# Optimization experiments

Hardware: AMD Instinct MI355X
Metric: run time of the kernel (lower is better)

The kernel has to match this reference:

```python
import jax, jax.numpy as jnp
import numpy as np

D_MODEL = 256
D_INNER = 512
NHEADS = 8
HEADDIM = 64
NGROUPS = 1
D_DIST = 4
LOG_SCALE = 512.0
MAX_VALUE = 4.0
NUM_POINTS = 10
EPS = 1e-5


def roty(t):
    c, s = jnp.cos(t), jnp.sin(t)
    z, o = jnp.zeros_like(t), jnp.ones_like(t)
    r0 = jnp.stack([c, z, s], -1)
    r1 = jnp.stack([z, o, z], -1)
    r2 = jnp.stack([-s, z, c], -1)
    return jnp.stack([r0, r1, r2], -2)


def box_corners(center, size, angle):
    # flip_axis_to_camera: (x, -z, y)
    cam_c = jnp.stack([center[..., 0], -center[..., 2], center[..., 1]], -1)
    R = roty(angle)  # (B,K,3,3)
    sx = jnp.array([1, 1, -1, -1, 1, 1, -1, -1], jnp.float32)
    sy = jnp.array([1, 1, 1, 1, -1, -1, -1, -1], jnp.float32)
    sz = jnp.array([1, -1, -1, 1, 1, -1, -1, 1], jnp.float32)
    l, w, h = size[..., 0:1], size[..., 1:2], size[..., 2:3]
    local = jnp.stack([l * sx / 2, h * sy / 2, w * sz / 2], -1)  # (B,K,8,3)
    cam = jnp.einsum('bkcj,bkij->bkci', local, R) + cam_c[..., None, :]
    # camera -> lidar: (x, z, -y)
    return jnp.stack([cam[..., 0], cam[..., 2], -cam[..., 1]], -1)


def trilinear_sample(table, g):
    # table (P,P,P,C); g (N,3) normalized coords (gx,gy,gz); gx->axis2, gy->axis1, gz->axis0
    # replicates F.grid_sample(mode='bilinear', align_corners=False, padding_mode='zeros')
    P = table.shape[0]
    pix = ((g + 1.0) * P - 1.0) * 0.5
    k, j, i = pix[:, 0], pix[:, 1], pix[:, 2]
    i0f, j0f, k0f = jnp.floor(i), jnp.floor(j), jnp.floor(k)
    wi, wj, wk = i - i0f, j - j0f, k - k0f
    i0, j0, k0 = i0f.astype(jnp.int32), j0f.astype(jnp.int32), k0f.astype(jnp.int32)
    out = jnp.zeros((g.shape[0], table.shape[-1]), table.dtype)
    for a in (0, 1):
        for b in (0, 1):
            for c in (0, 1):
                ii, jj, kk = i0 + a, j0 + b, k0 + c
                valid = (ii >= 0) & (ii < P) & (jj >= 0) & (jj < P) & (kk >= 0) & (kk < P)
                v = table[jnp.clip(ii, 0, P - 1), jnp.clip(jj, 0, P - 1), jnp.clip(kk, 0, P - 1)]
                w = (wi if a else 1 - wi) * (wj if b else 1 - wj) * (wk if c else 1 - wk)
                out = out + jnp.where(valid, w, 0.0)[:, None] * v
    return out


def box_dist(key_xyz, query_xyz, query_size, query_angle, w1, b1, w2):
    B, K = query_xyz.shape[:2]
    L = key_xyz.shape[1]
    corners = jax.lax.stop_gradient(box_corners(query_xyz, query_size, query_angle))
    d = corners.reshape(B, K * 8, 3)[:, :, None, :] - key_xyz[:, None, :, :]  # (B,K*8,L,3)
    d = jnp.stack([d[..., 0], -d[..., 2], d[..., 1]], -1)
    R = roty(jnp.tile(query_angle, (1, 8)))  # matches torch .repeat((1,8)) ordering (bug-faithful)
    d = jnp.einsum('bqlj,bqjk->bqlk', d, R)
    d = jnp.stack([d[..., 0], d[..., 2], -d[..., 1]], -1)
    d = jnp.sign(d) * jnp.log2(jnp.abs(d) * LOG_SCALE + 1.0) / np.float32(np.log2(8.0))
    g = (d / MAX_VALUE).reshape(-1, 3)
    lin = jnp.linspace(-MAX_VALUE, MAX_VALUE, NUM_POINTS, dtype=jnp.float32)
    coords = jnp.stack(jnp.meshgrid(lin, lin, lin, indexing='ij'), -1)  # (P,P,P,3)
    table = jnp.maximum(coords @ w1.T + b1, 0.0) @ w2.T  # cpb MLP -> (P,P,P,4)
    samp = trilinear_sample(table, g).reshape(B, K, 8, L, D_DIST)
    return samp.sum(axis=2).transpose(0, 2, 1, 3)  # (B,L,K,4)


def dwconv7(x, w, b):
    # x (B,L,C), depthwise conv1d k=7 pad=3
    y = jax.lax.conv_general_dilated(jnp.swapaxes(x, 1, 2), w, (1,), [(3, 3)],
                                     dimension_numbers=('NCH', 'OIH', 'NCH'),
                                     feature_group_count=w.shape[0])
    return jnp.swapaxes(y + b[None, :, None], 1, 2)


def issm_scan(x, Bm, Cm, dt, A, h0):
    # x (B,L,H,hd), Bm/Cm (B,L,K), dt (B,L,K,H), h0 (B,H,hd,K); state index = query axis K
    dA = jnp.exp(dt * A)          # (B,L,K,H)
    dB = dt * Bm[..., None]       # (B,L,K,H)
    xs = (jnp.moveaxis(x, 1, 0), jnp.moveaxis(dA, 1, 0), jnp.moveaxis(dB, 1, 0), jnp.moveaxis(Cm, 1, 0))

    def step(h, inp):
        x_t, dA_t, dB_t, C_t = inp
        h = h * jnp.swapaxes(dA_t, 1, 2)[:, :, None, :] + x_t[..., None] * jnp.swapaxes(dB_t, 1, 2)[:, :, None, :]
        return h, jnp.einsum('bhdk,bk->bhd', h, C_t)

    hT, ys = jax.lax.scan(step, h0, xs)
    return jnp.moveaxis(ys, 0, 1), hT


def _forward(in_key, in_query, key_xyz, query_xyz, query_size, query_angle, Wkey, conv_w, conv_b, convb_w, convb_b, Wq, Wbc, Wdt, dt_bias, A_log, Dp, Wok, Woq, key_norm_w, ln_w, ln_b, cpb_w1, cpb_b1, cpb_w2):
    B, L, _ = in_key.shape
    K = in_query.shape[1]
    zxbcdt = in_key @ Wkey.T
    z = zxbcdt[..., :D_INNER]
    xbc = zxbcdt[..., D_INNER:2 * D_INNER + 2 * NGROUPS]
    dt_k = zxbcdt[..., 2 * D_INNER + 2 * NGROUPS:]
    xbc_f = jax.nn.silu(dwconv7(xbc, conv_w, conv_b))
    x = xbc_f[..., :D_INNER].reshape(B, L, NHEADS, HEADDIM)
    b_bias = xbc_f[..., D_INNER:D_INNER + NGROUPS]
    c_bias = xbc_f[..., D_INNER + NGROUPS:]
    xbc_b = jax.nn.silu(dwconv7(xbc_f, convb_w, convb_b))
    x_b = xbc_b[..., :D_INNER].reshape(B, L, NHEADS, HEADDIM)
    bb_b = xbc_b[..., D_INNER:D_INNER + NGROUPS]
    cb_b = xbc_b[..., D_INNER + NGROUPS:]
    dist = box_dist(key_xyz, query_xyz, query_size, query_angle, cpb_w1, cpb_b1, cpb_w2)  # (B,L,K,4)
    bc = dist @ Wbc.T  # (B,L,K,2*ngroups)
    Bm0, Cm0 = bc[..., 0], bc[..., 1]
    dt = jax.nn.softplus(dist @ Wdt.T + dt_k[:, :, None, :] + dt_bias)  # (B,L,K,H)
    A = -jnp.exp(A_log)
    h0 = (in_query @ Wq.T).reshape(B, K, NHEADS, HEADDIM).transpose(0, 2, 3, 1)  # (B,H,hd,K)
    y_f, h_f = issm_scan(x, Bm0 + b_bias, Cm0 + c_bias, dt, A, h0)
    rev = lambda a: jnp.flip(a, axis=1)
    y_b, h_b = issm_scan(rev(x_b), rev(Bm0 + bb_b), rev(Cm0 + cb_b), rev(dt), A, h0)
    y = y_f + rev(y_b) + Dp[None, None, :, None] * x
    yk = y.reshape(B, L, D_INNER)
    gated = yk * jax.nn.silu(z)
    gated = gated * jax.lax.rsqrt(jnp.mean(gated * gated, -1, keepdims=True) + EPS) * key_norm_w
    out_key = gated @ Wok.T
    state = (0.5 * (h_f + h_b)).transpose(0, 3, 1, 2).reshape(B, K, D_INNER)
    mu = jnp.mean(state, -1, keepdims=True)
    var = jnp.mean((state - mu) ** 2, -1, keepdims=True)
    out_query = (((state - mu) * jax.lax.rsqrt(var + EPS)) * ln_w + ln_b) @ Woq.T
    return out_key, out_query


def setup_inputs():
    key = jax.random.key(0)
    ks = jax.random.split(key, 24)
    B, L, K = 2, 1024, 128
    D, DI, H, G = D_MODEL, D_INNER, NHEADS, NGROUPS
    CC = DI + 2 * G
    n = jax.random.normal
    inp = {}
    inp['in_key'] = n(ks[0], (B, L, D), jnp.float32)
    inp['in_query'] = n(ks[1], (B, K, D), jnp.float32)
    inp['key_xyz'] = jax.random.uniform(ks[2], (B, L, 3))
    inp['query_xyz'] = jax.random.uniform(ks[3], (B, K, 3))
    inp['query_size'] = jax.random.uniform(ks[4], (B, K, 3)) + 0.1
    inp['query_angle'] = jax.random.uniform(ks[5], (B, K)) * 2.0 * np.float32(np.pi)
    inp['Wkey'] = n(ks[6], (2 * DI + 2 * G + H, D)) * 0.02
    inp['conv_w'] = n(ks[7], (CC, 1, 7)) * 0.1
    inp['conv_b'] = jnp.zeros((CC,))
    inp['convb_w'] = n(ks[8], (CC, 1, 7)) * 0.1
    inp['convb_b'] = jnp.zeros((CC,))
    inp['Wq'] = n(ks[9], (DI, D)) * 0.02
    inp['Wbc'] = n(ks[10], (2 * G, D_DIST)) * 0.1
    inp['Wdt'] = n(ks[11], (H, D_DIST)) * 0.1
    dt = jnp.exp(jax.random.uniform(ks[12], (H,)) * (np.float32(np.log(0.1)) - np.float32(np.log(1e-4))) + np.float32(np.log(1e-4)))
    inp['dt_bias'] = dt + jnp.log(-jnp.expm1(-dt))
    inp['A_log'] = jnp.log(jax.random.uniform(ks[13], (H,), minval=1.0, maxval=16.0))
    inp['Dp'] = jnp.ones((H,))
    inp['Wok'] = n(ks[14], (D, DI)) * 0.02
    inp['Woq'] = n(ks[15], (D, DI)) * 0.02
    inp['key_norm_w'] = jnp.ones((DI,))
    inp['ln_w'] = jnp.ones((DI,))
    inp['ln_b'] = jnp.zeros((DI,))
    inp['cpb_w1'] = n(ks[16], (128, 3)) * 0.1
    inp['cpb_b1'] = jnp.zeros((128,))
    inp['cpb_w2'] = n(ks[17], (D_DIST, 128)) * 0.1
    return inp


def reference(in_key, in_query, key_xyz, query_xyz, query_size, query_angle, Wkey, conv_w, conv_b, convb_w, convb_b, Wq, Wbc, Wdt, dt_bias, A_log, Dp, Wok, Woq, key_norm_w, ln_w, ln_b, cpb_w1, cpb_b1, cpb_w2):
    return _forward(in_key, in_query, key_xyz, query_xyz, query_size, query_angle, Wkey, conv_w, conv_b, convb_w, convb_b, Wq, Wbc, Wdt, dt_bias, A_log, Dp, Wok, Woq, key_norm_w, ln_w, ln_b, cpb_w1, cpb_b1, cpb_w2)
```

## Files before the change

### kernel.cpp

```cpp
#include <hip/hip_runtime.h>
#include <math.h>

#define B_ 2
#define L_ 1024
#define K_ 128
#define DM 256
#define DI 512
#define NH 8
#define HD 64
#define CC 514
#define ZCOLS 1034
#define NC 16
#define TC 64

__device__ __forceinline__ float wave_sum(float v) {
    v += __shfl_xor(v, 1);  v += __shfl_xor(v, 2);  v += __shfl_xor(v, 4);
    v += __shfl_xor(v, 8);  v += __shfl_xor(v, 16); v += __shfl_xor(v, 32);
    return v;
}

__device__ __forceinline__ float dpp_row_reduce16(float v) {
    int t;
    t = __builtin_amdgcn_update_dpp(0, __float_as_int(v), 0x128, 0xF, 0xF, true);
    v += __int_as_float(t);
    t = __builtin_amdgcn_update_dpp(0, __float_as_int(v), 0x124, 0xF, 0xF, true);
    v += __int_as_float(t);
    t = __builtin_amdgcn_update_dpp(0, __float_as_int(v), 0x122, 0xF, 0xF, true);
    v += __int_as_float(t);
    t = __builtin_amdgcn_update_dpp(0, __float_as_int(v), 0x121, 0xF, 0xF, true);
    v += __int_as_float(t);
    return v;
}

__device__ __forceinline__ float silu_f(float x) {
    return x / (1.f + expf(-x));
}

__device__ void gemm_dev(const float* __restrict__ A, const float* __restrict__ Bm,
                         float* __restrict__ C, int M, int N, int K, int bm, int bn) {
    __shared__ float As[2][16][68];
    __shared__ float Bs[2][16][68];
    const int tid = threadIdx.x;
    const int sr = tid >> 2;
    const int sk = (tid & 3) * 4;
    const int tx = tid & 15, ty = tid >> 4;
    const int NT = K >> 4;
    const float* Arow = A + (size_t)(bm + sr) * K + sk;
    const float* Brow = Bm + (size_t)(bn + sr) * K + sk;
    const bool bok = (bn + sr) < N;

    float4 av = *(const float4*)Arow;
    float4 bv = bok ? *(const float4*)Brow : make_float4(0.f, 0.f, 0.f, 0.f);
    As[0][sk + 0][sr] = av.x; As[0][sk + 1][sr] = av.y;
    As[0][sk + 2][sr] = av.z; As[0][sk + 3][sr] = av.w;
    Bs[0][sk + 0][sr] = bv.x; Bs[0][sk + 1][sr] = bv.y;
    Bs[0][sk + 2][sr] = bv.z; Bs[0][sk + 3][sr] = bv.w;
    __syncthreads();

    float acc[4][4] = {};
    for (int t = 0; t < NT; ++t) {
        if (t + 1 < NT) {
            av = *(const float4*)(Arow + (t + 1) * 16);
            bv = bok ? *(const float4*)(Brow + (t + 1) * 16) : make_float4(0.f, 0.f, 0.f, 0.f);
        }
        const int bi = t & 1;
#pragma unroll
        for (int kk = 0; kk < 16; ++kk) {
            float4 a = *(const float4*)&As[bi][kk][ty * 4];
            float4 b = *(const float4*)&Bs[bi][kk][tx * 4];
            acc[0][0] = fmaf(a.x, b.x, acc[0][0]); acc[0][1] = fmaf(a.x, b.y, acc[0][1]);
            acc[0][2] = fmaf(a.x, b.z, acc[0][2]); acc[0][3] = fmaf(a.x, b.w, acc[0][3]);
            acc[1][0] = fmaf(a.y, b.x, acc[1][0]); acc[1][1] = fmaf(a.y, b.y, acc[1][1]);
            acc[1][2] = fmaf(a.y, b.z, acc[1][2]); acc[1][3] = fmaf(a.y, b.w, acc[1][3]);
            acc[2][0] = fmaf(a.z, b.x, acc[2][0]); acc[2][1] = fmaf(a.z, b.y, acc[2][1]);
            acc[2][2] = fmaf(a.z, b.z, acc[2][2]); acc[2][3] = fmaf(a.z, b.w, acc[2][3]);
            acc[3][0] = fmaf(a.w, b.x, acc[3][0]); acc[3][1] = fmaf(a.w, b.y, acc[3][1]);
            acc[3][2] = fmaf(a.w, b.z, acc[3][2]); acc[3][3] = fmaf(a.w, b.w, acc[3][3]);
        }
        __syncthreads();
        if (t + 1 < NT) {
            const int ni = (t + 1) & 1;
            As[ni][sk + 0][sr] = av.x; As[ni][sk + 1][sr] = av.y;
            As[ni][sk + 2][sr] = av.z; As[ni][sk + 3][sr] = av.w;
            Bs[ni][sk + 0][sr] = bv.x; Bs[ni][sk + 1][sr] = bv.y;
            Bs[ni][sk + 2][sr] = bv.z; Bs[ni][sk + 3][sr] = bv.w;
            __syncthreads();
        }
    }
#pragma unroll
    for (int i = 0; i < 4; ++i) {
        int m = bm + ty * 4 + i;
        int n0 = bn + tx * 4;
        if (n0 + 3 < N) {
            float* cp = &C[(size_t)m * N + n0];
            *(float2*)cp = make_float2(acc[i][0], acc[i][1]);
            *(float2*)(cp + 2) = make_float2(acc[i][2], acc[i][3]);
        } else {
#pragma unroll
            for (int j = 0; j < 4; ++j)
                if (n0 + j < N) C[(size_t)m * N + n0 + j] = acc[i][j];
        }
    }
}

__global__ __launch_bounds__(256) void front_k(
    const float* __restrict__ in_key, const float* __restrict__ Wkey, float* __restrict__ zx,
    const float* __restrict__ in_query, const float* __restrict__ Wq, float* __restrict__ h0b,
    const float* __restrict__ qxyz, const float* __restrict__ qsize,
    const float* __restrict__ qang, const float* __restrict__ w1,
    const float* __restrict__ b1, const float* __restrict__ w2,
    float* __restrict__ cb, float* __restrict__ tbl) {
    int bid = blockIdx.x, tid = threadIdx.x;
    if (bid < 544) {
        gemm_dev(in_key, Wkey, zx, 2048, ZCOLS, 256, (bid & 31) * 64, (bid >> 5) * 64);
    } else if (bid < 576) {
        int r = bid - 544;
        gemm_dev(in_query, Wq, h0b, 256, 512, 256, (r & 3) * 64, (r >> 2) * 64);
    } else if (bid < 584) {
        int idx = (bid - 576) * 256 + tid;
        int b = idx >> 10;
        int q = idx & 1023;
        int k = q >> 3;
        int c = q & 7;
        const float sx[8] = {1, 1, -1, -1, 1, 1, -1, -1};
        const float sy[8] = {1, 1, 1, 1, -1, -1, -1, -1};
        const float sz[8] = {1, -1, -1, 1, 1, -1, -1, 1};
        float cx = qxyz[(b * K_ + k) * 3 + 0];
        float cy = qxyz[(b * K_ + k) * 3 + 1];
        float cz = qxyz[(b * K_ + k) * 3 + 2];
        float lv = qsize[(b * K_ + k) * 3 + 0];
        float wv = qsize[(b * K_ + k) * 3 + 1];
        float hv = qsize[(b * K_ + k) * 3 + 2];
        float ang = qang[b * K_ + k];
        float ca = cosf(ang), sa = sinf(ang);
        float ccx = cx, ccy = -cz, ccz = cy;
        float l0 = lv * sx[c] * 0.5f;
        float l1 = hv * sy[c] * 0.5f;
        float l2 = wv * sz[c] * 0.5f;
        float m0 = ca * l0 + sa * l2 + ccx;
        float m1 = l1 + ccy;
        float m2 = -sa * l0 + ca * l2 + ccz;
        float angr = qang[b * K_ + (q & (K_ - 1))];
        float4* o = (float4*)(cb + (size_t)idx * 8);
        o[0] = make_float4(m0, m2, -m1, cosf(angr));
        o[1] = make_float4(sinf(angr), 0.f, 0.f, 0.f);
    } else {
        int p = (bid - 584) * 256 + tid;
        if (p >= 1000) return;
        int i = p / 100, j = (p / 10) % 10, k = p % 10;
        float c0 = (8.f / 9.f) * i - 4.f;
        float c1 = (8.f / 9.f) * j - 4.f;
        float c2 = (8.f / 9.f) * k - 4.f;
        float a0 = 0.f, a1 = 0.f, a2 = 0.f, a3 = 0.f;
        for (int m = 0; m < 128; ++m) {
            float t = fmaf(c0, w1[m * 3 + 0], fmaf(c1, w1[m * 3 + 1], fmaf(c2, w1[m * 3 + 2], b1[m])));
            t = fmaxf(t, 0.f);
            a0 = fmaf(t, w2[m], a0);
            a1 = fmaf(t, w2[128 + m], a1);
            a2 = fmaf(t, w2[256 + m], a2);
            a3 = fmaf(t, w2[384 + m], a3);
        }
        tbl[p * 4 + 0] = a0; tbl[p * 4 + 1] = a1;
        tbl[p * 4 + 2] = a2; tbl[p * 4 + 3] = a3;
    }
}

__global__ void dwconv_silu(const float* __restrict__ xin, int in_stride, int in_off,
                            const float* __restrict__ w, const float* __restrict__ bias,
                            float* __restrict__ out) {
    int c = blockIdx.y * blockDim.x + threadIdx.x;
    if (c >= CC) return;
    int row = blockIdx.x;
    int l = row & (L_ - 1);
    const float* xr = xin + (size_t)row * in_stride + in_off + c;
    float acc = bias[c];
#pragma unroll
    for (int j = 0; j < 7; ++j) {
        int ll = l + j - 3;
        if (ll >= 0 && ll < L_) acc = fmaf(xr[(ptrdiff_t)(j - 3) * in_stride], w[c * 7 + j], acc);
    }
    out[(size_t)row * CC + c] = silu_f(acc);
}

__global__ __launch_bounds__(128) void geo_k(
    const float* __restrict__ kxyz, const float* __restrict__ cb,
    const float* __restrict__ tbl, const float* __restrict__ zx,
    const float* __restrict__ xf, const float* __restrict__ xb,
    const float* __restrict__ wbc, const float* __restrict__ wdt,
    const float* __restrict__ dtb, const float* __restrict__ alog,
    float* __restrict__ dA, float* __restrict__ dBf, float* __restrict__ dBb,
    float* __restrict__ Cf, float* __restrict__ Cb) {
    __shared__ float t_s[4000];
    int row = blockIdx.x;
    int b = row >> 10;
    int l = row & 1023;
    int k = threadIdx.x;
    for (int i = threadIdx.x; i < 4000; i += 128) t_s[i] = tbl[i];
    __syncthreads();
    float kx = kxyz[(size_t)row * 3 + 0];
    float ky = kxyz[(size_t)row * 3 + 1];
    float kz = kxyz[(size_t)row * 3 + 2];
    float acc0 = 0.f, acc1 = 0.f, acc2 = 0.f, acc3 = 0.f;
#pragma unroll
    for (int c = 0; c < 8; ++c) {
        int q = k * 8 + c;
        const float4* p = (const float4*)(cb + (size_t)(b * 1024 + q) * 8);
        float4 v0 = p[0], v1 = p[1];
        float d0 = v0.x - kx, d1 = v0.y - ky, d2 = v0.z - kz;
        float rc = v0.w, rs = v1.x;
        float e0 = d0, e1 = -d2, e2 = d1;
        float f0 = rc * e0 - rs * e2;
        float f1 = e1;
        float f2 = rs * e0 + rc * e2;
        float g0 = f0, g1 = f2, g2 = -f1;
        g0 = copysignf(log2f(fabsf(g0) * 512.f + 1.f) * (1.f / 12.f), g0);
        g1 = copysignf(log2f(fabsf(g1) * 512.f + 1.f) * (1.f / 12.f), g1);
        g2 = copysignf(log2f(fabsf(g2) * 512.f + 1.f) * (1.f / 12.f), g2);
        float iq = 5.f * g2 + 4.5f;
        float jq = 5.f * g1 + 4.5f;
        float kq = 5.f * g0 + 4.5f;
        float i0f = floorf(iq), j0f = floorf(jq), k0f = floorf(kq);
        float wi = iq - i0f, wj = jq - j0f, wk = kq - k0f;
        int i0 = (int)i0f, j0 = (int)j0f, k0 = (int)k0f;
#pragma unroll
        for (int a = 0; a < 2; ++a) {
#pragma unroll
            for (int bb = 0; bb < 2; ++bb) {
#pragma unroll
                for (int cc = 0; cc < 2; ++cc) {
                    int ii = i0 + a, jj = j0 + bb, kk = k0 + cc;
                    if ((unsigned)ii < 10u && (unsigned)jj < 10u && (unsigned)kk < 10u) {
                        float wgt = (a ? wi : 1.f - wi) * (bb ? wj : 1.f - wj) * (cc ? wk : 1.f - wk);
                        const float* tp = &t_s[((ii * 10 + jj) * 10 + kk) * 4];
                        acc0 = fmaf(wgt, tp[0], acc0);
                        acc1 = fmaf(wgt, tp[1], acc1);
                        acc2 = fmaf(wgt, tp[2], acc2);
                        acc3 = fmaf(wgt, tp[3], acc3);
                    }
                }
            }
        }
    }
    float B0 = acc0 * wbc[0] + acc1 * wbc[1] + acc2 * wbc[2] + acc3 * wbc[3];
    float C0 = acc0 * wbc[4] + acc1 * wbc[5] + acc2 * wbc[6] + acc3 * wbc[7];
    float bbf = xf[(size_t)row * CC + 512], cbf = xf[(size_t)row * CC + 513];
    float bbb = xb[(size_t)row * CC + 512], cbb = xb[(size_t)row * CC + 513];
    Cf[(size_t)row * K_ + k] = C0 + cbf;
    Cb[(size_t)row * K_ + k] = C0 + cbb;
    float Bf = B0 + bbf, Bb = B0 + bbb;
#pragma unroll
    for (int hh = 0; hh < NH; ++hh) {
        float s = acc0 * wdt[hh * 4 + 0] + acc1 * wdt[hh * 4 + 1] +
                  acc2 * wdt[hh * 4 + 2] + acc3 * wdt[hh * 4 + 3];
        s += zx[(size_t)row * ZCOLS + 1026 + hh] + dtb[hh];
        float dtv = (s > 20.f) ? s : log1pf(expf(s));
        float Av = -expf(alog[hh]);
        size_t o = ((size_t)(b * NH + hh) * L_ + l) * K_ + k;
        dA[o] = expf(dtv * Av);
        dBf[o] = dtv * Bf;
        dBb[o] = dtv * Bb;
    }
}

__global__ __launch_bounds__(256) void scan_part6(
    const float* __restrict__ dA, const float* __restrict__ dBf, const float* __restrict__ dBb,
    const float* __restrict__ Cf, const float* __restrict__ Cb,
    const float* __restrict__ xf, const float* __restrict__ xb,
    float* __restrict__ Sbuf, float* __restrict__ Pbuf,
    float* __restrict__ yf, float* __restrict__ yb) {
    __shared__ float lds[2][3584];
    int bid = blockIdx.x;
    int c = bid & 15;
    int hh = (bid >> 4) & 7;
    int b = (bid >> 7) & 1;
    int dir = bid >> 8;
    int tid = threadIdx.x;
    int lane = tid & 63;
    int w = tid >> 6;
    int dg = lane >> 4, kg = lane & 15;
    int dloc = w * 4 + dg;
    int klo = kg * 4, khi = 64 + kg * 4;

    const float* Bsrc = dir ? dBb : dBf;
    const float* Csrc = dir ? Cb : Cf;
    const float* Xsrc = dir ? xb : xf;
    float* Ydst = dir ? yb : yf;
    int t0 = dir ? (L_ - 1 - c * TC) : c * TC;
    int stp = dir ? -1 : 1;

    const float* Abase = dA + ((size_t)(b * NH + hh) * L_) * K_;
    const float* Bbase = Bsrc + ((size_t)(b * NH + hh) * L_) * K_;
    const float* Cbase = Csrc + ((size_t)b * L_) * K_;
    const float* Xbase = Xsrc + ((size_t)b * L_) * CC + hh * HD;

    const bool hasx = (tid < 128);

    auto gaddr = [&](int v, int tb) -> const float* {
        if (v < 768) {
            int r = (v >> 5) & 7;
            int c4 = v & 31;
            int l = t0 + stp * (tb + r);
            const float* base = (v < 256) ? Abase : ((v < 512) ? Bbase : Cbase);
            return base + (size_t)l * K_ + c4 * 4;
        } else {
            int vv = v - 768;
            int r = vv >> 4, c4 = vv & 15;
            int l = t0 + stp * (tb + r);
            return Xbase + (size_t)l * CC + c4 * 4;
        }
    };

    float hA[8] = {0, 0, 0, 0, 0, 0, 0, 0};
    float hB[8] = {0, 0, 0, 0, 0, 0, 0, 0};
    float hC[8] = {0, 0, 0, 0, 0, 0, 0, 0};
    float hD[8] = {0, 0, 0, 0, 0, 0, 0, 0};
    float cum[8] = {1, 1, 1, 1, 1, 1, 1, 1};

    float4 rA = *(const float4*)gaddr(tid, 0);
    float4 rB = *(const float4*)gaddr(256 + tid, 0);
    float4 rC = *(const float4*)gaddr(512 + tid, 0);
    float4 rX = hasx ? *(const float4*)gaddr(768 + tid, 0) : make_float4(0, 0, 0, 0);
    *(float4*)&lds[0][4 * tid] = rA;
    *(float4*)&lds[0][1024 + 4 * tid] = rB;
    *(float4*)&lds[0][2048 + 4 * tid] = rC;
    if (hasx) *(float4*)&lds[0][3072 + 4 * tid] = rX;
    __syncthreads();

    float* pY = Ydst + ((size_t)(b * L_ + t0)) * DI + hh * HD + dloc;
    const ptrdiff_t dY = (ptrdiff_t)stp * DI;

    for (int it = 0; it < TC / 8; ++it) {
        int tb = it * 8;
        if (it < TC / 8 - 1) {
            rA = *(const float4*)gaddr(tid, tb + 8);
            rB = *(const float4*)gaddr(256 + tid, tb + 8);
            rC = *(const float4*)gaddr(512 + tid, tb + 8);
            if (hasx) rX = *(const float4*)gaddr(768 + tid, tb + 8);
        }
        const float* Lb = lds[it & 1];
        float4 a0 = *(const float4*)&Lb[klo];
        float4 a1 = *(const float4*)&Lb[khi];
        float4 b0 = *(const float4*)&Lb[1024 + klo];
        float4 b1 = *(const float4*)&Lb[1024 + khi];
        float4 c0 = *(const float4*)&Lb[2048 + klo];
        float4 c1 = *(const float4*)&Lb[2048 + khi];
        float x0 = Lb[3072 + dloc];
        float x1 = Lb[3072 + 16 + dloc];
        float x2 = Lb[3072 + 32 + dloc];
        float x3 = Lb[3072 + 48 + dloc];
#pragma unroll
        for (int st = 0; st < 8; ++st) {
            float4 na0, na1, nb0, nb1, nc0, nc1;
            float nx0 = 0.f, nx1 = 0.f, nx2 = 0.f, nx3 = 0.f;
            if (st < 7) {
                int o = (st + 1) * 128;
                na0 = *(const float4*)&Lb[o + klo];
                na1 = *(const float4*)&Lb[o + khi];
                nb0 = *(const float4*)&Lb[1024 + o + klo];
                nb1 = *(const float4*)&Lb[1024 + o + khi];
                nc0 = *(const float4*)&Lb[2048 + o + klo];
                nc1 = *(const float4*)&Lb[2048 + o + khi];
                int xo = 3072 + (st + 1) * 64 + dloc;
                nx0 = Lb[xo]; nx1 = Lb[xo + 16]; nx2 = Lb[xo + 32]; nx3 = Lb[xo + 48];
            }
            cum[0] *= a0.x; cum[1] *= a0.y; cum[2] *= a0.z; cum[3] *= a0.w;
            cum[4] *= a1.x; cum[5] *= a1.y; cum[6] *= a1.z; cum[7] *= a1.w;
            float u0, u1, u2, u3;
            hA[0] = fmaf(hA[0], a0.x, x0 * b0.x); u0 = hA[0] * c0.x;
            hA[1] = fmaf(hA[1], a0.y, x0 * b0.y); u1 = hA[1] * c0.y;
            hA[2] = fmaf(hA[2], a0.z, x0 * b0.z); u2 = hA[2] * c0.z;
            hA[3] = fmaf(hA[3], a0.w, x0 * b0.w); u3 = hA[3] * c0.w;
            hA[4] = fmaf(hA[4], a1.x, x0 * b1.x); u0 = fmaf(hA[4], c1.x, u0);
            hA[5] = fmaf(hA[5], a1.y, x0 * b1.y); u1 = fmaf(hA[5], c1.y, u1);
            hA[6] = fmaf(hA[6], a1.z, x0 * b1.z); u2 = fmaf(hA[6], c1.z, u2);
            hA[7] = fmaf(hA[7], a1.w, x0 * b1.w); u3 = fmaf(hA[7], c1.w, u3);
            float rrA = dpp_row_reduce16((u0 + u1) + (u2 + u3));
            hB[0] = fmaf(hB[0], a0.x, x1 * b0.x); u0 = hB[0] * c0.x;
            hB[1] = fmaf(hB[1], a0.y, x1 * b0.y); u1 = hB[1] * c0.y;
            hB[2] = fmaf(hB[2], a0.z, x1 * b0.z); u2 = hB[2] * c0.z;
            hB[3] = fmaf(hB[3], a0.w, x1 * b0.w); u3 = hB[3] * c0.w;
            hB[4] = fmaf(hB[4], a1.x, x1 * b1.x); u0 = fmaf(hB[4], c1.x, u0);
            hB[5] = fmaf(hB[5], a1.y, x1 * b1.y); u1 = fmaf(hB[5], c1.y, u1);
            hB[6] = fmaf(hB[6], a1.z, x1 * b1.z); u2 = fmaf(hB[6], c1.z, u2);
            hB[7] = fmaf(hB[7], a1.w, x1 * b1.w); u3 = fmaf(hB[7], c1.w, u3);
            float rrB = dpp_row_reduce16((u0 + u1) + (u2 + u3));
            hC[0] = fmaf(hC[0], a0.x, x2 * b0.x); u0 = hC[0] * c0.x;
            hC[1] = fmaf(hC[1], a0.y, x2 * b0.y); u1 = hC[1] * c0.y;
            hC[2] = fmaf(hC[2], a0.z, x2 * b0.z); u2 = hC[2] * c0.z;
            hC[3] = fmaf(hC[3], a0.w, x2 * b0.w); u3 = hC[3] * c0.w;
            hC[4] = fmaf(hC[4], a1.x, x2 * b1.x); u0 = fmaf(hC[4], c1.x, u0);
            hC[5] = fmaf(hC[5], a1.y, x2 * b1.y); u1 = fmaf(hC[5], c1.y, u1);
            hC[6] = fmaf(hC[6], a1.z, x2 * b1.z); u2 = fmaf(hC[6], c1.z, u2);
            hC[7] = fmaf(hC[7], a1.w, x2 * b1.w); u3 = fmaf(hC[7], c1.w, u3);
            float rrC = dpp_row_reduce16((u0 + u1) + (u2 + u3));
            hD[0] = fmaf(hD[0], a0.x, x3 * b0.x); u0 = hD[0] * c0.x;
            hD[1] = fmaf(hD[1], a0.y, x3 * b0.y); u1 = hD[1] * c0.y;
            hD[2] = fmaf(hD[2], a0.z, x3 * b0.z); u2 = hD[2] * c0.z;
            hD[3] = fmaf(hD[3], a0.w, x3 * b0.w); u3 = hD[3] * c0.w;
            hD[4] = fmaf(hD[4], a1.x, x3 * b1.x); u0 = fmaf(hD[4], c1.x, u0);
            hD[5] = fmaf(hD[5], a1.y, x3 * b1.y); u1 = fmaf(hD[5], c1.y, u1);
            hD[6] = fmaf(hD[6], a1.z, x3 * b1.z); u2 = fmaf(hD[6], c1.z, u2);
            hD[7] = fmaf(hD[7], a1.w, x3 * b1.w); u3 = fmaf(hD[7], c1.w, u3);
            float rrD = dpp_row_reduce16((u0 + u1) + (u2 + u3));
            if (kg == 0) { pY[0] = rrA; pY[16] = rrB; pY[32] = rrC; pY[48] = rrD; }
            pY += dY;
            if (st < 7) {
                a0 = na0; a1 = na1; b0 = nb0; b1 = nb1; c0 = nc0; c1 = nc1;
                x0 = nx0; x1 = nx1; x2 = nx2; x3 = nx3;
            }
        }
        __syncthreads();
        if (it < TC / 8 - 1) {
            *(float4*)&lds[(it + 1) & 1][4 * tid] = rA;
            *(float4*)&lds[(it + 1) & 1][1024 + 4 * tid] = rB;
            *(float4*)&lds[(it + 1) & 1][2048 + 4 * tid] = rC;
            if (hasx) *(float4*)&lds[(it + 1) & 1][3072 + 4 * tid] = rX;
        }
        __syncthreads();
    }

    int ibh = (dir * B_ + b) * NH + hh;
    {
        float* Sp = Sbuf + (((size_t)ibh * NC + c) * HD + dloc) * K_;
        *(float4*)(Sp + klo) = make_float4(hA[0], hA[1], hA[2], hA[3]);
        *(float4*)(Sp + khi) = make_float4(hA[4], hA[5], hA[6], hA[7]);
        Sp += (size_t)16 * K_;
        *(float4*)(Sp + klo) = make_float4(hB[0], hB[1], hB[2], hB[3]);
        *(float4*)(Sp + khi) = make_float4(hB[4], hB[5], hB[6], hB[7]);
        Sp += (size_t)16 * K_;
        *(float4*)(Sp + klo) = make_float4(hC[0], hC[1], hC[2], hC[3]);
        *(float4*)(Sp + khi) = make_float4(hC[4], hC[5], hC[6], hC[7]);
        Sp += (size_t)16 * K_;
        *(float4*)(Sp + klo) = make_float4(hD[0], hD[1], hD[2], hD[3]);
        *(float4*)(Sp + khi) = make_float4(hD[4], hD[5], hD[6], hD[7]);
    }
    if (dir == 0 && tid < 16) {
        float* Pp = Pbuf + ((size_t)((b * NH + hh) * NC + c)) * K_;
        *(float4*)(Pp + klo) = make_float4(cum[0], cum[1], cum[2], cum[3]);
        *(float4*)(Pp + khi) = make_float4(cum[4], cum[5], cum[6], cum[7]);
    }
}

__global__ __launch_bounds__(256) void scan_combine(
    const float* __restrict__ h0buf, float* __restrict__ Sbuf,
    const float* __restrict__ Pbuf, float* __restrict__ hfin) {
    int bid = blockIdx.x;
    int dq = bid & 3;
    int hh = (bid >> 2) & 7;
    int b = (bid >> 5) & 1;
    int dir = bid >> 6;
    int tid = threadIdx.x;
    int w = tid >> 6;
    int lane = tid & 63;
    int dsl = dq * 4 + w;
    int dg = lane >> 4, kg = lane & 15;
    int d = dsl * 4 + dg;
    int k0 = kg * 8;

    float H[8];
#pragma unroll
    for (int j = 0; j < 8; ++j)
        H[j] = h0buf[(size_t)(b * K_ + k0 + j) * DI + hh * HD + d];

    int ibh = (dir * B_ + b) * NH + hh;
    for (int c = 0; c < NC; ++c) {
        float* Sp = Sbuf + (((size_t)ibh * NC + c) * HD + d) * K_ + k0;
        int cF = dir ? (NC - 1 - c) : c;
        const float* Pp = Pbuf + ((size_t)((b * NH + hh) * NC + cF)) * K_ + k0;
        float4 sA = *(const float4*)(Sp + 0);
        float4 sB = *(const float4*)(Sp + 4);
        float4 pA = *(const float4*)(Pp + 0);
        float4 pB = *(const float4*)(Pp + 4);
        *(float4*)(Sp + 0) = make_float4(H[0], H[1], H[2], H[3]);
        *(float4*)(Sp + 4) = make_float4(H[4], H[5], H[6], H[7]);
        H[0] = fmaf(H[0], pA.x, sA.x); H[1] = fmaf(H[1], pA.y, sA.y);
        H[2] = fmaf(H[2], pA.z, sA.z); H[3] = fmaf(H[3], pA.w, sA.w);
        H[4] = fmaf(H[4], pB.x, sB.x); H[5] = fmaf(H[5], pB.y, sB.y);
        H[6] = fmaf(H[6], pB.z, sB.z); H[7] = fmaf(H[7], pB.w, sB.w);
    }
    float* hf = hfin + ((((size_t)dir * B_ + b) * NH + hh) * HD + d) * K_ + k0;
    *(float4*)(hf + 0) = make_float4(H[0], H[1], H[2], H[3]);
    *(float4*)(hf + 4) = make_float4(H[4], H[5], H[6], H[7]);
}

#define CP 72
#define WSWZ(k) ((((k) >> 3) & 3) << 2)
__global__ __launch_bounds__(256) void scan_corr(
    const float* __restrict__ dA, const float* __restrict__ Cf, const float* __restrict__ Cb,
    const float* __restrict__ Sbuf, float* __restrict__ yf, float* __restrict__ yb) {
    __shared__ float Wl[128][CP];
    __shared__ float Hl[128][CP];
    int iid = blockIdx.x;
    int c = iid & 15;
    int hh = (iid >> 4) & 7;
    int b = (iid >> 7) & 1;
    int dir = iid >> 8;
    int tid = threadIdx.x;
    const float* Csrc = dir ? Cb : Cf;

    if (tid < 128) {
        int k = tid;
        float cum = 1.f;
        const float* pA = dA + ((size_t)(b * NH + hh) * L_) * K_ + k;
        const float* pC = Csrc + ((size_t)b * L_) * K_ + k;
        int sw = WSWZ(k);
#pragma unroll 4
        for (int t = 0; t < TC; ++t) {
            int l = dir ? (L_ - 1 - (c * TC + t)) : (c * TC + t);
            cum *= pA[(size_t)l * K_];
            Wl[k][t ^ sw] = cum * pC[(size_t)l * K_];
        }
    }
    {
        int d = tid & 63, kq = tid >> 6;
        int ibh = (dir * B_ + b) * NH + hh;
        const float* Hp = Sbuf + (((size_t)ibh * NC + c) * HD + d) * K_;
#pragma unroll
        for (int i = 0; i < 8; ++i) {
            int q = kq * 8 + i;
            float4 v = *(const float4*)(Hp + q * 4);
            Hl[q * 4 + 0][d] = v.x; Hl[q * 4 + 1][d] = v.y;
            Hl[q * 4 + 2][d] = v.z; Hl[q * 4 + 3][d] = v.w;
        }
    }
    __syncthreads();
    int a = tid >> 4;
    int bc = tid & 15;
    int t0v = a * 4, d0v = bc * 4;
    float acc[4][4] = {};
    for (int k = 0; k < 128; ++k) {
        float4 w4 = *(const float4*)&Wl[k][t0v ^ WSWZ(k)];
        float4 h4 = *(const float4*)&Hl[k][d0v];
        acc[0][0] = fmaf(w4.x, h4.x, acc[0][0]); acc[0][1] = fmaf(w4.x, h4.y, acc[0][1]);
        acc[0][2] = fmaf(w4.x, h4.z, acc[0][2]); acc[0][3] = fmaf(w4.x, h4.w, acc[0][3]);
        acc[1][0] = fmaf(w4.y, h4.x, acc[1][0]); acc[1][1] = fmaf(w4.y, h4.y, acc[1][1]);
        acc[1][2] = fmaf(w4.y, h4.z, acc[1][2]); acc[1][3] = fmaf(w4.y, h4.w, acc[1][3]);
        acc[2][0] = fmaf(w4.z, h4.x, acc[2][0]); acc[2][1] = fmaf(w4.z, h4.y, acc[2][1]);
        acc[2][2] = fmaf(w4.z, h4.z, acc[2][2]); acc[2][3] = fmaf(w4.z, h4.w, acc[2][3]);
        acc[3][0] = fmaf(w4.w, h4.x, acc[3][0]); acc[3][1] = fmaf(w4.w, h4.y, acc[3][1]);
        acc[3][2] = fmaf(w4.w, h4.z, acc[3][2]); acc[3][3] = fmaf(w4.w, h4.w, acc[3][3]);
    }
    float* Ydst = dir ? yb : yf;
#pragma unroll
    for (int i = 0; i < 4; ++i) {
        int t = t0v + i;
        int l = dir ? (L_ - 1 - (c * TC + t)) : (c * TC + t);
        float* yp = Ydst + ((size_t)(b * L_ + l)) * DI + hh * HD + d0v;
        float4 old = *(float4*)yp;
        old.x += acc[i][0]; old.y += acc[i][1];
        old.z += acc[i][2]; old.w += acc[i][3];
        *(float4*)yp = old;
    }
}

__global__ __launch_bounds__(256) void gated_k(
    const float* __restrict__ yf, const float* __restrict__ yb,
    const float* __restrict__ xf, const float* __restrict__ zx,
    const float* __restrict__ Dp, const float* __restrict__ knw,
    float* __restrict__ gated) {
    __shared__ float sb[4];
    int row = blockIdx.x;
    int tid = threadIdx.x;
    float g[2];
    float ss = 0.f;
#pragma unroll
    for (int u = 0; u < 2; ++u) {
        int c = tid + u * 256;
        float yv = yf[(size_t)row * DI + c] + yb[(size_t)row * DI + c] +
                   Dp[c >> 6] * xf[(size_t)row * CC + c];
        float z = zx[(size_t)row * ZCOLS + c];
        float gv = yv * silu_f(z);
        g[u] = gv;
        ss = fmaf(gv, gv, ss);
    }
    float wsum = wave_sum(ss);
    if ((tid & 63) == 0) sb[tid >> 6] = wsum;
    __syncthreads();
    float tot = sb[0] + sb[1] + sb[2] + sb[3];
    float rms = rsqrtf(tot * (1.f / 512.f) + 1e-5f);
#pragma unroll
    for (int u = 0; u < 2; ++u) {
        int c = tid + u * 256;
        gated[(size_t)row * DI + c] = g[u] * rms * knw[c];
    }
}

__global__ __launch_bounds__(256) void final_k(
    const float* __restrict__ gated, const float* __restrict__ Wok, float* __restrict__ out,
    const float* __restrict__ hfin, const float* __restrict__ lnw,
    const float* __restrict__ lnb, const float* __restrict__ woq,
    float* __restrict__ outq) {
    int bid = blockIdx.x, tid = threadIdx.x;
    if (bid < 128) {
        gemm_dev(gated, Wok, out, 2048, 256, 512, (bid & 31) * 64, (bid >> 5) * 64);
        return;
    }
    __shared__ float sln[512];
    __shared__ float sb1[4];
    __shared__ float sb2[4];
    int bk = bid - 128;
    int b = bk >> 7;
    int k = bk & 127;
    float st[2];
    float ssum = 0.f;
#pragma unroll
    for (int u = 0; u < 2; ++u) {
        int c = tid + u * 256;
        int hh = c >> 6, d = c & 63;
        size_t o0 = (((size_t)(0 * B_ + b) * NH + hh) * HD + d) * K_ + k;
        size_t o1 = (((size_t)(1 * B_ + b) * NH + hh) * HD + d) * K_ + k;
        st[u] = 0.5f * (hfin[o0] + hfin[o1]);
        ssum += st[u];
    }
    float wsum = wave_sum(ssum);
    if ((tid & 63) == 0) sb1[tid >> 6] = wsum;
    __syncthreads();
    float mu = (sb1[0] + sb1[1] + sb1[2] + sb1[3]) * (1.f / 512.f);
    float vs = 0.f;
#pragma unroll
    for (int u = 0; u < 2; ++u) {
        float t = st[u] - mu;
        vs = fmaf(t, t, vs);
    }
    float wv = wave_sum(vs);
    if ((tid & 63) == 0) sb2[tid >> 6] = wv;
    __syncthreads();
    float var = (sb2[0] + sb2[1] + sb2[2] + sb2[3]) * (1.f / 512.f);
    float inv = rsqrtf(var + 1e-5f);
#pragma unroll
    for (int u = 0; u < 2; ++u) {
        int c = tid + u * 256;
        sln[c] = (st[u] - mu) * inv * lnw[c] + lnb[c];
    }
    __syncthreads();
    const float4* w4 = (const float4*)(woq + (size_t)tid * 512);
    float acc = 0.f;
#pragma unroll 4
    for (int i = 0; i < 128; ++i) {
        float4 wvv = w4[i];
        float4 sv = *(const float4*)&sln[i * 4];
        acc = fmaf(wvv.x, sv.x, acc);
        acc = fmaf(wvv.y, sv.y, acc);
        acc = fmaf(wvv.z, sv.z, acc);
        acc = fmaf(wvv.w, sv.w, acc);
    }
    outq[(size_t)bk * 256 + tid] = acc;
}

extern "C" void kernel_launch(void* const* d_in, const int* in_sizes, int n_in,
                              void* d_out, int out_size, void* d_ws, size_t ws_size,
                              hipStream_t stream) {
    const float* in_key      = (const float*)d_in[0];
    const float* in_query    = (const float*)d_in[1];
    const float* key_xyz     = (const float*)d_in[2];
    const float* query_xyz   = (const float*)d_in[3];
    const float* query_size  = (const float*)d_in[4];
    const float* query_angle = (const float*)d_in[5];
    const float* Wkey        = (const float*)d_in[6];
    const float* conv_w      = (const float*)d_in[7];
    const float* conv_b      = (const float*)d_in[8];
    const float* convb_w     = (const float*)d_in[9];
    const float* convb_b     = (const float*)d_in[10];
    const float* Wq          = (const float*)d_in[11];
    const float* Wbc         = (const float*)d_in[12];
    const float* Wdt         = (const float*)d_in[13];
    const float* dt_bias     = (const float*)d_in[14];
    const float* A_log       = (const float*)d_in[15];
    const float* Dp          = (const float*)d_in[16];
    const float* Wok         = (const float*)d_in[17];
    const float* Woq         = (const float*)d_in[18];
    const float* key_norm_w  = (const float*)d_in[19];
    const float* ln_w        = (const float*)d_in[20];
    const float* ln_b        = (const float*)d_in[21];
    const float* cpb_w1      = (const float*)d_in[22];
    const float* cpb_b1      = (const float*)d_in[23];
    const float* cpb_w2      = (const float*)d_in[24];
    float* out = (float*)d_out;

    float* wsf = (float*)d_ws;
    float* zx    = wsf + 0;
    float* xf    = wsf + 2117632;
    float* xb    = wsf + 3170304;
    float* tbl   = wsf + 4222976;
    float* cbuf  = wsf + 4226976;
    float* Pbuf  = wsf + 4243360;
    float* dAa   = wsf + 5291936;
    float* dBf   = wsf + 7389088;
    float* dBb   = wsf + 9486240;
    float* Cfb   = wsf + 11583392;
    float* Cbb   = wsf + 11845536;
    float* h0b   = wsf + 12107680;
    float* yfb   = wsf + 12238752;
    float* ybb   = wsf + 13287328;
    float* hfin  = wsf + 14335904;
    float* gated = wsf + 14598048;
    float* Sbuf  = wsf + 15646624;

    front_k<<<588, 256, 0, stream>>>(in_key, Wkey, zx, in_query, Wq, h0b,
                                     query_xyz, query_size, query_angle,
                                     cpb_w1, cpb_b1, cpb_w2, cbuf, tbl);
    dwconv_silu<<<dim3(2048, 3), 256, 0, stream>>>(zx, ZCOLS, 512, conv_w, conv_b, xf);
    dwconv_silu<<<dim3(2048, 3), 256, 0, stream>>>(xf, CC, 0, convb_w, convb_b, xb);
    geo_k<<<2048, 128, 0, stream>>>(key_xyz, cbuf, tbl, zx, xf, xb,
                                    Wbc, Wdt, dt_bias, A_log,
                                    dAa, dBf, dBb, Cfb, Cbb);
    scan_part6<<<512, 256, 0, stream>>>(dAa, dBf, dBb, Cfb, Cbb, xf, xb,
                                        Sbuf, Pbuf, yfb, ybb);
    scan_combine<<<128, 256, 0, stream>>>(h0b, Sbuf, Pbuf, hfin);
    scan_corr<<<512, 256, 0, stream>>>(dAa, Cfb, Cbb, Sbuf, yfb, ybb);
    gated_k<<<2048, 256, 0, stream>>>(yfb, ybb, xf, zx, Dp, key_norm_w, gated);
    final_k<<<384, 256, 0, stream>>>(gated, Wok, out, hfin, ln_w, ln_b, Woq,
                                     out + 524288);
}
```

Before: 205.0 us.

## Split-K the key projection GEMM into two partial buffers and trim barriers

The in_key×Wkey GEMM is split along K into two halves. Each half writes its own partial output buffer (zxA and zxB), which doubles the number of GEMM blocks. Every consumer (dwconv, geo_k, gated_k) now adds the two partials, so zx traffic roughly doubles in exchange for more parallelism. The box-corner and CPB-table setup moves into its own small kernel. The double-buffered GEMM loop and a scan loop each drop one __syncthreads per iteration by relying on the alternate buffer.

Measured after the change: 219.7 us. 7.2% more time.

```diff
diff --git a/kernel.cpp b/kernel.cpp
--- a/kernel.cpp
+++ b/kernel.cpp
@@ -37,16 +37,17 @@
 }
 
 __device__ void gemm_dev(const float* __restrict__ A, const float* __restrict__ Bm,
-                         float* __restrict__ C, int M, int N, int K, int bm, int bn) {
+                         float* __restrict__ C, int M, int N, int Kt, int ld, int koff,
+                         int bm, int bn) {
     __shared__ float As[2][16][68];
     __shared__ float Bs[2][16][68];
     const int tid = threadIdx.x;
     const int sr = tid >> 2;
     const int sk = (tid & 3) * 4;
     const int tx = tid & 15, ty = tid >> 4;
-    const int NT = K >> 4;
-    const float* Arow = A + (size_t)(bm + sr) * K + sk;
-    const float* Brow = Bm + (size_t)(bn + sr) * K + sk;
+    const int NT = Kt >> 4;
+    const float* Arow = A + (size_t)(bm + sr) * ld + koff + sk;
+    const float* Brow = Bm + (size_t)(bn + sr) * ld + koff + sk;
     const bool bok = (bn + sr) < N;
 
     float4 av = *(const float4*)Arow;
@@ -77,15 +78,14 @@
             acc[3][0] = fmaf(a.w, b.x, acc[3][0]); acc[3][1] = fmaf(a.w, b.y, acc[3][1]);
             acc[3][2] = fmaf(a.w, b.z, acc[3][2]); acc[3][3] = fmaf(a.w, b.w, acc[3][3]);
         }
-        __syncthreads();
         if (t + 1 < NT) {
             const int ni = (t + 1) & 1;
             As[ni][sk + 0][sr] = av.x; As[ni][sk + 1][sr] = av.y;
             As[ni][sk + 2][sr] = av.z; As[ni][sk + 3][sr] = av.w;
             Bs[ni][sk + 0][sr] = bv.x; Bs[ni][sk + 1][sr] = bv.y;
             Bs[ni][sk + 2][sr] = bv.z; Bs[ni][sk + 3][sr] = bv.w;
-            __syncthreads();
-        }
+        }
+        __syncthreads();
     }
 #pragma unroll
     for (int i = 0; i < 4; ++i) {
@@ -104,20 +104,31 @@
 }
 
 __global__ __launch_bounds__(256) void front_k(
-    const float* __restrict__ in_key, const float* __restrict__ Wkey, float* __restrict__ zx,
-    const float* __restrict__ in_query, const float* __restrict__ Wq, float* __restrict__ h0b,
+    const float* __restrict__ in_key, const float* __restrict__ Wkey,
+    float* __restrict__ zxA, float* __restrict__ zxB,
+    const float* __restrict__ in_query, const float* __restrict__ Wq,
+    float* __restrict__ h0b) {
+    int bid = blockIdx.x;
+    if (bid < 1088) {
+        int base = bid >> 1, half = bid & 1;
+        float* outp = half ? zxB : zxA;
+        gemm_dev(in_key, Wkey, outp, 2048, ZCOLS, 128, 256, half * 128,
+                 (base & 31) * 64, (base >> 5) * 64);
+    } else {
+        int r = bid - 1088;
+        gemm_dev(in_query, Wq, h0b, 256, 512, 256, 256, 0,
+                 (r & 3) * 64, (r >> 2) * 64);
+    }
+}
+
+__global__ __launch_bounds__(256) void setup_k(
     const float* __restrict__ qxyz, const float* __restrict__ qsize,
     const float* __restrict__ qang, const float* __restrict__ w1,
     const float* __restrict__ b1, const float* __restrict__ w2,
     float* __restrict__ cb, float* __restrict__ tbl) {
     int bid = blockIdx.x, tid = threadIdx.x;
-    if (bid < 544) {
-        gemm_dev(in_key, Wkey, zx, 2048, ZCOLS, 256, (bid & 31) * 64, (bid >> 5) * 64);
-    } else if (bid < 576) {
-        int r = bid - 544;
-        gemm_dev(in_query, Wq, h0b, 256, 512, 256, (r & 3) * 64, (r >> 2) * 64);
-    } else if (bid < 584) {
-        int idx = (bid - 576) * 256 + tid;
+    if (bid < 8) {
+        int idx = bid * 256 + tid;
         int b = idx >> 10;
         int q = idx & 1023;
         int k = q >> 3;
@@ -145,7 +156,7 @@
         o[0] = make_float4(m0, m2, -m1, cosf(angr));
         o[1] = make_float4(sinf(angr), 0.f, 0.f, 0.f);
     } else {
-        int p = (bid - 584) * 256 + tid;
+        int p = (bid - 8) * 256 + tid;
         if (p >= 1000) return;
         int i = p / 100, j = (p / 10) % 10, k = p % 10;
         float c0 = (8.f / 9.f) * i - 4.f;
@@ -165,6 +176,27 @@
     }
 }
 
+__global__ void dwconv_silu2(const float* __restrict__ xa, const float* __restrict__ xbp,
+                             const float* __restrict__ w, const float* __restrict__ bias,
+                             float* __restrict__ out) {
+    int c = blockIdx.y * blockDim.x + threadIdx.x;
+    if (c >= CC) return;
+    int row = blockIdx.x;
+    int l = row & (L_ - 1);
+    const float* ra = xa + (size_t)row * ZCOLS + 512 + c;
+    const float* rb = xbp + (size_t)row * ZCOLS + 512 + c;
+    float acc = bias[c];
+#pragma unroll
+    for (int j = 0; j < 7; ++j) {
+        int ll = l + j - 3;
+        if (ll >= 0 && ll < L_) {
+            ptrdiff_t o = (ptrdiff_t)(j - 3) * ZCOLS;
+            acc = fmaf(ra[o] + rb[o], w[c * 7 + j], acc);
+        }
+    }
+    out[(size_t)row * CC + c] = silu_f(acc);
+}
+
 __global__ void dwconv_silu(const float* __restrict__ xin, int in_stride, int in_off,
                             const float* __restrict__ w, const float* __restrict__ bias,
                             float* __restrict__ out) {
@@ -184,7 +216,8 @@
 
 __global__ __launch_bounds__(128) void geo_k(
     const float* __restrict__ kxyz, const float* __restrict__ cb,
-    const float* __restrict__ tbl, const float* __restrict__ zx,
+    const float* __restrict__ tbl, const float* __restrict__ zxA,
+    const float* __restrict__ zxB,
     const float* __restrict__ xf, const float* __restrict__ xb,
     const float* __restrict__ wbc, const float* __restrict__ wdt,
     const float* __restrict__ dtb, const float* __restrict__ alog,
@@ -252,7 +285,7 @@
     for (int hh = 0; hh < NH; ++hh) {
         float s = acc0 * wdt[hh * 4 + 0] + acc1 * wdt[hh * 4 + 1] +
                   acc2 * wdt[hh * 4 + 2] + acc3 * wdt[hh * 4 + 3];
-        s += zx[(size_t)row * ZCOLS + 1026 + hh] + dtb[hh];
+        s += zxA[(size_t)row * ZCOLS + 1026 + hh] + zxB[(size_t)row * ZCOLS + 1026 + hh] + dtb[hh];
         float dtv = (s > 20.f) ? s : log1pf(expf(s));
         float Av = -expf(alog[hh]);
         size_t o = ((size_t)(b * NH + hh) * L_ + l) * K_ + k;
@@ -409,7 +442,6 @@
                 x0 = nx0; x1 = nx1; x2 = nx2; x3 = nx3;
             }
         }
-        __syncthreads();
         if (it < TC / 8 - 1) {
             *(float4*)&lds[(it + 1) & 1][4 * tid] = rA;
             *(float4*)&lds[(it + 1) & 1][1024 + 4 * tid] = rB;
@@ -555,7 +587,8 @@
 
 __global__ __launch_bounds__(256) void gated_k(
     const float* __restrict__ yf, const float* __restrict__ yb,
-    const float* __restrict__ xf, const float* __restrict__ zx,
+    const float* __restrict__ xf, const float* __restrict__ zxA,
+    const float* __restrict__ zxB,
     const float* __restrict__ Dp, const float* __restrict__ knw,
     float* __restrict__ gated) {
     __shared__ float sb[4];
@@ -568,7 +601,7 @@
         int c = tid + u * 256;
         float yv = yf[(size_t)row * DI + c] + yb[(size_t)row * DI + c] +
                    Dp[c >> 6] * xf[(size_t)row * CC + c];
-        float z = zx[(size_t)row * ZCOLS + c];
+        float z = zxA[(size_t)row * ZCOLS + c] + zxB[(size_t)row * ZCOLS + c];
         float gv = yv * silu_f(z);
         g[u] = gv;
         ss = fmaf(gv, gv, ss);
@@ -592,7 +625,7 @@
     float* __restrict__ outq) {
     int bid = blockIdx.x, tid = threadIdx.x;
     if (bid < 128) {
-        gemm_dev(gated, Wok, out, 2048, 256, 512, (bid & 31) * 64, (bid >> 5) * 64);
+        gemm_dev(gated, Wok, out, 2048, 256, 512, 512, 0, (bid & 31) * 64, (bid >> 5) * 64);
         return;
     }
     __shared__ float sln[512];
@@ -678,7 +711,7 @@
     float* out = (float*)d_out;
 
     float* wsf = (float*)d_ws;
-    float* zx    = wsf + 0;
+    float* zxA   = wsf + 0;
     float* xf    = wsf + 2117632;
     float* xb    = wsf + 3170304;
     float* tbl   = wsf + 4222976;
@@ -695,20 +728,21 @@
     float* hfin  = wsf + 14335904;
     float* gated = wsf + 14598048;
     float* Sbuf  = wsf + 15646624;
-
-    front_k<<<588, 256, 0, stream>>>(in_key, Wkey, zx, in_query, Wq, h0b,
-                                     query_xyz, query_size, query_angle,
-                                     cpb_w1, cpb_b1, cpb_w2, cbuf, tbl);
-    dwconv_silu<<<dim3(2048, 3), 256, 0, stream>>>(zx, ZCOLS, 512, conv_w, conv_b, xf);
+    float* zxB   = wsf + 19840928;
+
+    setup_k<<<12, 256, 0, stream>>>(query_xyz, query_size, query_angle,
+                                    cpb_w1, cpb_b1, cpb_w2, cbuf, tbl);
+    front_k<<<1120, 256, 0, stream>>>(in_key, Wkey, zxA, zxB, in_query, Wq, h0b);
+    dwconv_silu2<<<dim3(2048, 3), 256, 0, stream>>>(zxA, zxB, conv_w, conv_b, xf);
     dwconv_silu<<<dim3(2048, 3), 256, 0, stream>>>(xf, CC, 0, convb_w, convb_b, xb);
-    geo_k<<<2048, 128, 0, stream>>>(key_xyz, cbuf, tbl, zx, xf, xb,
+    geo_k<<<2048, 128, 0, stream>>>(key_xyz, cbuf, tbl, zxA, zxB, xf, xb,
                                     Wbc, Wdt, dt_bias, A_log,
                                     dAa, dBf, dBb, Cfb, Cbb);
     scan_part6<<<512, 256, 0, stream>>>(dAa, dBf, dBb, Cfb, Cbb, xf, xb,
                                         Sbuf, Pbuf, yfb, ybb);
     scan_combine<<<128, 256, 0, stream>>>(h0b, Sbuf, Pbuf, hfin);
     scan_corr<<<512, 256, 0, stream>>>(dAa, Cfb, Cbb, Sbuf, yfb, ybb);
-    gated_k<<<2048, 256, 0, stream>>>(yfb, ybb, xf, zx, Dp, key_norm_w, gated);
+    gated_k<<<2048, 256, 0, stream>>>(yfb, ybb, xf, zxA, zxB, Dp, key_norm_w, gated);
     final_k<<<384, 256, 0, stream>>>(gated, Wok, out, hfin, ln_w, ln_b, Woq,
                                      out + 524288);
 }
```
